# Kernel optimization log

Measured on AMD Instinct MI355X. Metric: run time of the kernel, lower is better.

The kernel has to match this reference:

```python
import jax, jax.numpy as jnp
import numpy as np

OCC_W, SMOOTH_W, SPARSE_W, CONS_W = 1.0, 0.1, 0.01, 0.1
EPS = 1e-7  # torch BCE clamps log terms; clip preds for numerical parity


def setup_inputs() -> dict:
    key = jax.random.key(0)
    k1, k2, k3, k4 = jax.random.split(key, 4)
    N, F = 16384, 64
    predictions = jax.random.uniform(k1, (N,), dtype=jnp.float32, minval=1e-4, maxval=1.0 - 1e-4)
    targets = jax.random.uniform(k2, (N,), dtype=jnp.float32)
    features = jax.random.normal(k3, (N, F), dtype=jnp.float32)
    points = jax.random.normal(k4, (N, 3), dtype=jnp.float32)
    return {"predictions": predictions, "targets": targets, "features": features, "points": points}


def reference(predictions, targets, features, points):
    # --- occupancy loss: BCE(mean) ---
    p = jnp.clip(predictions, EPS, 1.0 - EPS)
    occupancy = -jnp.mean(targets * jnp.log(p) + (1.0 - targets) * jnp.log1p(-p))

    # --- smoothness loss: for each point, 3 nearest neighbors (excl. self) ---
    # Fused all-pairs sq-distance [N, N] + top-k, replacing the per-point python loop.
    sq = jnp.sum(points * points, axis=1)                      # [N]
    d2 = sq[:, None] + sq[None, :] - 2.0 * (points @ points.T)  # [N, N]
    d2 = jnp.maximum(d2, 0.0)  # monotone in distance, so ordering == torch.norm ordering
    _, idx = jax.lax.top_k(-d2, 4)                              # 4 smallest distances
    nn_idx = idx[:, 1:4]                                        # drop self (index 0)
    # per-point local gradient: mean |pred_i - pred_nn|, then mean over points
    smoothness = jnp.mean(jnp.abs(predictions[:, None] - predictions[nn_idx]))

    # --- sparsity loss: mean |features| ---
    sparsity = jnp.mean(jnp.abs(features))

    # --- consistency loss: MSE ---
    consistency = jnp.mean((predictions - targets) ** 2)

    total = (OCC_W * occupancy + SMOOTH_W * smoothness
             + SPARSE_W * sparsity + CONS_W * consistency)
    return total
```

## Files before the change

### kernel.cpp

```cpp
#include <hip/hip_runtime.h>
#include <float.h>
#include <math.h>


constexpr int   N_ = 16384;
constexpr int   F_ = 64;
constexpr float OCC_W = 1.0f, SMOOTH_W = 0.1f, SPARSE_W = 0.01f, CONS_W = 0.1f;
constexpr float EPS_ = 1e-7f;

constexpr int CHUNKS  = 16;
constexpr int CHUNK_J = N_ / CHUNKS;
constexpr int JTILES  = CHUNK_J / 32;
constexpr int IB      = 128;
constexpr int IBLOCKS = N_ / IB;

typedef __attribute__((ext_vector_type(8)))  short bf16x8;
typedef __attribute__((ext_vector_type(16))) float f32x16;

union U128 { uint4 u; bf16x8 s; };

__device__ __forceinline__ void ins4f(float t, float& b0, float& b1, float& b2, float& b3) {
  float n0 = fminf(b0, t);
  float n1 = __builtin_amdgcn_fmed3f(b0, b1, t);
  float n2 = __builtin_amdgcn_fmed3f(b1, b2, t);
  float n3 = __builtin_amdgcn_fmed3f(b2, b3, t);
  b0 = n0; b1 = n1; b2 = n2; b3 = n3;
}

__device__ __forceinline__ void split2(float x, unsigned& h16, unsigned& l16) {
  unsigned u = __float_as_uint(x);
  unsigned r = u + 0x7FFFu + ((u >> 16) & 1u);
  h16 = r >> 16;
  float lo = x - __uint_as_float(r & 0xFFFF0000u);
  unsigned v = __float_as_uint(lo);
  l16 = (v + 0x7FFFu + ((v >> 16) & 1u)) >> 16;
}


__global__ __launch_bounds__(256) void knn_mfma(const float* __restrict__ pts,
                                                float4* __restrict__ cand,
                                                unsigned* __restrict__ done) {
  if (blockIdx.x == 0 && threadIdx.x == 0) *done = 0u;
  __shared__ uint4 AF[2][CHUNK_J];
  const int tid   = threadIdx.x;
  const int chunk = blockIdx.x & (CHUNKS - 1);
  const int ibk   = blockIdx.x >> 4;
  const int j0    = chunk * CHUNK_J;

  for (int t = tid; t < CHUNK_J; t += 256) {
    int j = j0 + t;
    float qx = pts[3 * j], qy = pts[3 * j + 1], qz = pts[3 * j + 2];
    float w  = fmaf(qx, qx, fmaf(qy, qy, qz * qz));
    unsigned Hx, Lx, Hy, Ly, Hz, Lz, Hw, Lw;
    split2(-2.f * qx, Hx, Lx);
    split2(-2.f * qy, Hy, Ly);
    split2(-2.f * qz, Hz, Lz);
    split2(w, Hw, Lw);
    AF[0][t] = make_uint4(Hx | (Hx << 16), Lx | (Lx << 16),
                          Hy | (Hy << 16), Ly | (Ly << 16));
    AF[1][t] = make_uint4(Hz | (Hz << 16), Lz | (Lz << 16),
                          Hw | (Lw << 16), 0u);
  }

  const int lane = tid & 63, wv = tid >> 6;
  const int h = lane >> 5, il = lane & 31;
  const int i = ibk * IB + wv * 32 + il;
  U128 bf;
  {
    float x = pts[3 * i], y = pts[3 * i + 1], z = pts[3 * i + 2];
    unsigned hx, lx, hy, ly, hz, lz;
    split2(x, hx, lx);
    split2(y, hy, ly);
    split2(z, hz, lz);
    if (h == 0) {
      unsigned a = hx | (lx << 16), b = hy | (ly << 16);
      bf.u = make_uint4(a, a, b, b);
    } else {
      unsigned a = hz | (lz << 16);
      bf.u = make_uint4(a, a, 0x3F803F80u, 0u);
    }
  }
  __syncthreads();

  float b0 = FLT_MAX, b1 = FLT_MAX, b2 = FLT_MAX, b3 = FLT_MAX;
  const f32x16 zacc = {};
  const unsigned qb0 = (unsigned)(chunk * 256 + h);
  const uint4* __restrict__ afp = &AF[h][0];

#pragma unroll 4
  for (int t = 0; t < JTILES; ++t) {
    U128 af; af.u = afp[t * 32 + il];
    f32x16 acc = __builtin_amdgcn_mfma_f32_32x32x16_bf16(af.s, bf.s, zacc, 0, 0, 0);
    unsigned q = qb0 + (unsigned)(t * 8);
#pragma unroll
    for (int g = 0; g < 4; ++g) {
      float m = fminf(fminf(acc[4 * g + 0], acc[4 * g + 1]),
                      fminf(acc[4 * g + 2], acc[4 * g + 3]));
      float kf = __uint_as_float((__float_as_uint(m) & 0xFFFFF000u) | (q + 2u * g));
      ins4f(kf, b0, b1, b2, b3);
    }
  }

  float o0 = __shfl_xor(b0, 32), o1 = __shfl_xor(b1, 32),
        o2 = __shfl_xor(b2, 32), o3 = __shfl_xor(b3, 32);
  ins4f(o0, b0, b1, b2, b3);
  ins4f(o1, b0, b1, b2, b3);
  ins4f(o2, b0, b1, b2, b3);
  ins4f(o3, b0, b1, b2, b3);
  if (h == 0) cand[(size_t)chunk * N_ + i] = make_float4(b0, b1, b2, b3);
}

__global__ __launch_bounds__(256) void merge_kernel(const float* __restrict__ pred,
                                                    const float* __restrict__ targ,
                                                    const float* __restrict__ feat,
                                                    const float* __restrict__ pts,
                                                    const float4* __restrict__ cand,
                                                    float4* __restrict__ part,
                                                    unsigned* __restrict__ done,
                                                    float* __restrict__ out) {
  __shared__ float4 sh[256];
  __shared__ float ws4[4][4];
  __shared__ int is_last;
  constexpr int CPT = CHUNKS / 4;
  int tid  = threadIdx.x;
  int lane = tid & 63;
  int sub  = tid >> 6;
  int i = blockIdx.x * 64 + lane;

  const float4* f4 = (const float4*)feat;
  float s_sp = 0.f;
#pragma unroll
  for (int s = 0; s < 4; ++s) {
    float4 v = f4[(size_t)s * 65536 + blockIdx.x * 256 + tid];
    s_sp += fabsf(v.x) + fabsf(v.y) + fabsf(v.z) + fabsf(v.w);
  }

  float b0 = FLT_MAX, b1 = FLT_MAX, b2 = FLT_MAX, b3 = FLT_MAX;
#pragma unroll
  for (int cc = 0; cc < CPT; ++cc) {
    float4 v = cand[(size_t)(sub * CPT + cc) * N_ + i];
    ins4f(v.x, b0, b1, b2, b3);
    ins4f(v.y, b0, b1, b2, b3);
    ins4f(v.z, b0, b1, b2, b3);
    ins4f(v.w, b0, b1, b2, b3);
  }
  sh[tid] = make_float4(b0, b1, b2, b3);
  __syncthreads();

  float s_occ = 0.f, s_cons = 0.f, s_sm = 0.f;
  if (sub == 0) {
#pragma unroll
    for (int w = 1; w < 4; ++w) {
      float4 v = sh[w * 64 + lane];
      ins4f(v.x, b0, b1, b2, b3);
      ins4f(v.y, b0, b1, b2, b3);
      ins4f(v.z, b0, b1, b2, b3);
      ins4f(v.w, b0, b1, b2, b3);
    }
    unsigned qarr[4] = {__float_as_uint(b0) & 0xFFFu, __float_as_uint(b1) & 0xFFFu,
                        __float_as_uint(b2) & 0xFFFu, __float_as_uint(b3) & 0xFFFu};
    float xi = pts[3 * i], yi = pts[3 * i + 1], zi = pts[3 * i + 2];
    float c0 = FLT_MAX, c1 = FLT_MAX, c2 = FLT_MAX;
    float p0 = 0.f, p1 = 0.f, p2 = 0.f;
#pragma unroll
    for (int s = 0; s < 4; ++s) {
#pragma unroll
      for (int m = 0; m < 4; ++m) {
        int j = (int)(qarr[s] * 4 + m);
        float dx = xi - pts[3 * j], dy = yi - pts[3 * j + 1], dz = zi - pts[3 * j + 2];
        float d2 = fmaf(dx, dx, fmaf(dy, dy, dz * dz));
        float pj = pred[j];
        if (j != i && d2 < c2) {
          bool cc0 = d2 < c0, cc1 = d2 < c1;
          float n2 = cc1 ? c1 : d2;               float m2 = cc1 ? p1 : pj;
          float n1 = cc0 ? c0 : (cc1 ? d2 : c1);  float m1 = cc0 ? p0 : (cc1 ? pj : p1);
          float n0 = cc0 ? d2 : c0;               float m0 = cc0 ? pj : p0;
          c0 = n0; c1 = n1; c2 = n2; p0 = m0; p1 = m1; p2 = m2;
        }
      }
    }
    float pi = pred[i], tg = targ[i];
    float p  = fminf(fmaxf(pi, EPS_), 1.0f - EPS_);
    s_occ  = -(tg * __logf(p) + (1.0f - tg) * __logf(1.0f - p));
    float dd = pi - tg;
    s_cons = dd * dd;
    s_sm   = fabsf(pi - p0) + fabsf(pi - p1) + fabsf(pi - p2);
  }

  for (int off = 32; off > 0; off >>= 1) {
    s_sp   += __shfl_down(s_sp, off);
    s_occ  += __shfl_down(s_occ, off);
    s_cons += __shfl_down(s_cons, off);
    s_sm   += __shfl_down(s_sm, off);
  }
  if ((tid & 63) == 0) {
    int w = tid >> 6;
    ws4[w][0] = s_occ; ws4[w][1] = s_cons; ws4[w][2] = s_sp; ws4[w][3] = s_sm;
  }
  __syncthreads();
  if (tid == 0) {
    part[blockIdx.x] = make_float4(ws4[0][0] + ws4[1][0] + ws4[2][0] + ws4[3][0],
                                   ws4[0][1] + ws4[1][1] + ws4[2][1] + ws4[3][1],
                                   ws4[0][2] + ws4[1][2] + ws4[2][2] + ws4[3][2],
                                   ws4[0][3] + ws4[1][3] + ws4[2][3] + ws4[3][3]);
    __threadfence();
    unsigned prev = atomicAdd(done, 1u);
    is_last = (prev == (unsigned)(gridDim.x - 1));
  }
  __syncthreads();

  if (is_last) {
    __threadfence();
    float4 a = part[tid];
    float o = a.x, cn = a.y, sp = a.z, sm = a.w;
    for (int off = 32; off > 0; off >>= 1) {
      o  += __shfl_down(o, off);
      cn += __shfl_down(cn, off);
      sp += __shfl_down(sp, off);
      sm += __shfl_down(sm, off);
    }
    if ((tid & 63) == 0) {
      int w = tid >> 6;
      ws4[w][0] = o; ws4[w][1] = cn; ws4[w][2] = sp; ws4[w][3] = sm;
    }
    __syncthreads();
    if (tid == 0) {
      float occ  = ws4[0][0] + ws4[1][0] + ws4[2][0] + ws4[3][0];
      float cons = ws4[0][1] + ws4[1][1] + ws4[2][1] + ws4[3][1];
      float spar = ws4[0][2] + ws4[1][2] + ws4[2][2] + ws4[3][2];
      float smoo = ws4[0][3] + ws4[1][3] + ws4[2][3] + ws4[3][3];
      out[0] = OCC_W * (occ / (float)N_)
             + CONS_W * (cons / (float)N_)
             + SPARSE_W * (spar / (float)(N_ * F_))
             + SMOOTH_W * (smoo / (float)(N_ * 3));
    }
  }
}

extern "C" void kernel_launch(void* const* d_in, const int* in_sizes, int n_in,
                              void* d_out, int out_size, void* d_ws, size_t ws_size,
                              hipStream_t stream) {
  const float* pred = (const float*)d_in[0];
  const float* targ = (const float*)d_in[1];
  const float* feat = (const float*)d_in[2];
  const float* pts  = (const float*)d_in[3];
  float* out = (float*)d_out;

  char*     ws   = (char*)d_ws;
  float4*   part = (float4*)ws;
  unsigned* done = (unsigned*)(ws + 4096);
  float4*   cand = (float4*)(ws + 8192);

  knn_mfma<<<IBLOCKS * CHUNKS, 256, 0, stream>>>(pts, cand, done);
  merge_kernel<<<256, 256, 0, stream>>>(pred, targ, feat, pts, cand, part, done, out);
}
```

Baseline: 103.0 us.

## Coarsen top-k candidate groups to 16 columns to halve scan inserts

The MFMA scan now reduces 8 accumulator values per group, covering 16 candidate columns across both half-waves, and inserts 2 keys per tile instead of 4. The index field embedded in the low bits shrinks to 10 bits. A deduplicating merge across the half-wave shuffle is added, because both halves now tag the same group IDs. The refinement stage then evaluates 16 exact distances per candidate group instead of 4. This cuts the inner-loop insert work and costs more gather and distance work in the merge kernel, plus coarser key quantization.

```diff
diff --git a/kernel.cpp b/kernel.cpp
--- a/kernel.cpp
+++ b/kernel.cpp
@@ -84,29 +84,51 @@
 
   float b0 = FLT_MAX, b1 = FLT_MAX, b2 = FLT_MAX, b3 = FLT_MAX;
   const f32x16 zacc = {};
-  const unsigned qb0 = (unsigned)(chunk * 256 + h);
+  const unsigned idb = (unsigned)(chunk * (CHUNK_J / 16));
   const uint4* __restrict__ afp = &AF[h][0];
 
 #pragma unroll 4
   for (int t = 0; t < JTILES; ++t) {
     U128 af; af.u = afp[t * 32 + il];
     f32x16 acc = __builtin_amdgcn_mfma_f32_32x32x16_bf16(af.s, bf.s, zacc, 0, 0, 0);
-    unsigned q = qb0 + (unsigned)(t * 8);
-#pragma unroll
-    for (int g = 0; g < 4; ++g) {
-      float m = fminf(fminf(acc[4 * g + 0], acc[4 * g + 1]),
-                      fminf(acc[4 * g + 2], acc[4 * g + 3]));
-      float kf = __uint_as_float((__float_as_uint(m) & 0xFFFFF000u) | (q + 2u * g));
-      ins4f(kf, b0, b1, b2, b3);
-    }
+    float m0 = fminf(fminf(fminf(acc[0], acc[1]), fminf(acc[2], acc[3])),
+                     fminf(fminf(acc[4], acc[5]), fminf(acc[6], acc[7])));
+    float k0 = __uint_as_float((__float_as_uint(m0) & 0xFFFFFC00u) | (idb + 2u * t));
+    ins4f(k0, b0, b1, b2, b3);
+    float m1 = fminf(fminf(fminf(acc[8], acc[9]), fminf(acc[10], acc[11])),
+                     fminf(fminf(acc[12], acc[13]), fminf(acc[14], acc[15])));
+    float k1 = __uint_as_float((__float_as_uint(m1) & 0xFFFFFC00u) | (idb + 2u * t + 1u));
+    ins4f(k1, b0, b1, b2, b3);
   }
 
   float o0 = __shfl_xor(b0, 32), o1 = __shfl_xor(b1, 32),
         o2 = __shfl_xor(b2, 32), o3 = __shfl_xor(b3, 32);
-  ins4f(o0, b0, b1, b2, b3);
-  ins4f(o1, b0, b1, b2, b3);
-  ins4f(o2, b0, b1, b2, b3);
-  ins4f(o3, b0, b1, b2, b3);
+  {
+    float B[4] = {b0, b1, b2, b3};
+    float O[4] = {o0, o1, o2, o3};
+    unsigned ibd[4], iod[4];
+#pragma unroll
+    for (int k = 0; k < 4; ++k) {
+      ibd[k] = __float_as_uint(B[k]) & 0x3FFu;
+      iod[k] = __float_as_uint(O[k]) & 0x3FFu;
+    }
+#pragma unroll
+    for (int k = 0; k < 4; ++k) {
+#pragma unroll
+      for (int m = 0; m < 4; ++m) {
+        bool dup = (iod[k] == ibd[m]);
+        bool om  = dup && (O[k] >= B[m]);
+        bool bm  = dup && (O[k] <  B[m]);
+        if (om) O[k] = FLT_MAX;
+        if (bm) B[m] = FLT_MAX;
+      }
+    }
+    b0 = b1 = b2 = b3 = FLT_MAX;
+#pragma unroll
+    for (int k = 0; k < 4; ++k) ins4f(B[k], b0, b1, b2, b3);
+#pragma unroll
+    for (int k = 0; k < 4; ++k) ins4f(O[k], b0, b1, b2, b3);
+  }
   if (h == 0) cand[(size_t)chunk * N_ + i] = make_float4(b0, b1, b2, b3);
 }
 
@@ -157,16 +179,16 @@
       ins4f(v.z, b0, b1, b2, b3);
       ins4f(v.w, b0, b1, b2, b3);
     }
-    unsigned qarr[4] = {__float_as_uint(b0) & 0xFFFu, __float_as_uint(b1) & 0xFFFu,
-                        __float_as_uint(b2) & 0xFFFu, __float_as_uint(b3) & 0xFFFu};
+    unsigned qarr[4] = {__float_as_uint(b0) & 0x3FFu, __float_as_uint(b1) & 0x3FFu,
+                        __float_as_uint(b2) & 0x3FFu, __float_as_uint(b3) & 0x3FFu};
     float xi = pts[3 * i], yi = pts[3 * i + 1], zi = pts[3 * i + 2];
     float c0 = FLT_MAX, c1 = FLT_MAX, c2 = FLT_MAX;
     float p0 = 0.f, p1 = 0.f, p2 = 0.f;
 #pragma unroll
     for (int s = 0; s < 4; ++s) {
-#pragma unroll
-      for (int m = 0; m < 4; ++m) {
-        int j = (int)(qarr[s] * 4 + m);
+#pragma unroll 8
+      for (int m = 0; m < 16; ++m) {
+        int j = (int)(qarr[s] * 16 + m);
         float dx = xi - pts[3 * j], dy = yi - pts[3 * j + 1], dz = zi - pts[3 * j + 2];
         float d2 = fmaf(dx, dx, fmaf(dy, dy, dz * dz));
         float pj = pred[j];
```

Result: slower. 112.0 us (+8.8%).
